# Kernel tuning notes

Hardware: AMD Instinct MI355X
Metric: run time of the kernel (lower is better)

Reference implementation:

```python
import jax, jax.numpy as jnp
import numpy as np

RADIUS = 0.2
NSAMPLE = 32
USE_XYZ = True


def setup_inputs() -> dict:
    key = jax.random.key(0)
    k1, k2, k3 = jax.random.split(key, 3)
    B, N, S, C = 8, 16384, 1024, 64
    xyz = jax.random.uniform(k1, (B, N, 3), dtype=jnp.float32)
    new_xyz = jax.random.uniform(k2, (B, S, 3), dtype=jnp.float32)
    features = jax.random.normal(k3, (B, C, N), dtype=jnp.float32)
    return {"xyz": xyz, "new_xyz": new_xyz, "features": features}


def _ball_query(xyz, new_xyz, radius, nsample):
    """For each query point, the first `nsample` point indices within `radius`,
    padded with the first valid index (0 if none) — matches the CUDA kernel."""
    B, N, _ = xyz.shape
    # squared distances [B, S, N]
    d2 = jnp.sum((new_xyz[:, :, None, :] - xyz[:, None, :, :]) ** 2, axis=-1)
    within = d2 < (radius * radius)
    # encode: valid points keep their index, invalid get sentinel N; sorting
    # then yields the first-in-order valid indices, as the CUDA kernel does.
    keys = jnp.where(within, jnp.arange(N, dtype=jnp.int32)[None, None, :], N)
    idx = jnp.sort(keys, axis=-1)[:, :, :nsample]          # [B, S, K]
    first = idx[:, :, 0:1]
    first = jnp.where(first < N, first, 0)                 # no neighbor -> 0
    idx = jnp.where(idx < N, idx, first)
    return idx.astype(jnp.int32)


def reference(xyz, new_xyz, features):
    idx = _ball_query(xyz, new_xyz, RADIUS, NSAMPLE)       # [B, S, K] int32
    # group xyz: gather [B, S, K, 3] then center on new_xyz
    grouped_xyz = jnp.take_along_axis(xyz[:, None, :, :], idx[:, :, :, None], axis=2)
    grouped_xyz = grouped_xyz - new_xyz[:, :, None, :]
    grouped_xyz = jnp.transpose(grouped_xyz, (0, 3, 1, 2))  # [B, 3, S, K]
    # group features: [B, C, 1, N] gathered with [B, 1, S, K] -> [B, C, S, K]
    grouped_feats = jnp.take_along_axis(features[:, :, :, None].transpose(0, 1, 3, 2),
                                        idx[:, None, :, :], axis=3)
    if USE_XYZ:
        return jnp.concatenate([grouped_xyz, grouped_feats], axis=1)  # [B, 3+C, S, K]
    return grouped_feats
```

## Files before the change

kernel.cpp:

```cpp
#include <hip/hip_runtime.h>


#define BB 8
#define NN 16384
#define SS 1024
#define CC 64
#define NSAMP 32
#define OUTCH (3 + CC)

#define R2 0.04f

__global__ __launch_bounds__(256) void query_kernel(
    const float* __restrict__ xyz,
    const float* __restrict__ new_xyz,
    int* __restrict__ idxq,
    float* __restrict__ out)
{
    __shared__ int sidx[4][NSAMP];

    const int t    = threadIdx.x;
    const int wave = t >> 6;
    const int lane = t & 63;
    const int q    = blockIdx.x * 4 + wave;
    const int b    = q >> 10;
    const int s    = q & (SS - 1);

    const float* xb = xyz + (size_t)b * NN * 3;
    const float qx = new_xyz[((size_t)b * SS + s) * 3 + 0];
    const float qy = new_xyz[((size_t)b * SS + s) * 3 + 1];
    const float qz = new_xyz[((size_t)b * SS + s) * 3 + 2];
    const unsigned long long below = (1ull << lane) - 1ull;

    int count = 0;
    for (int base = 0; base < NN; base += 512) {
        float d2[8];
        #pragma unroll
        for (int j = 0; j < 8; ++j) {
            const int i = base + j * 64 + lane;
            const float dx = qx - xb[i * 3 + 0];
            const float dy = qy - xb[i * 3 + 1];
            const float dz = qz - xb[i * 3 + 2];
            d2[j] = __fadd_rn(__fadd_rn(__fmul_rn(dx, dx),
                                        __fmul_rn(dy, dy)),
                              __fmul_rn(dz, dz));
        }
        #pragma unroll
        for (int j = 0; j < 8; ++j) {
            const bool within = d2[j] < R2;
            const unsigned long long m = __ballot(within);
            if (within) {
                const int pos = count + __popcll(m & below);
                if (pos < NSAMP) sidx[wave][pos] = base + j * 64 + lane;
            }
            count += __popcll(m);
        }
        if (count >= NSAMP) break;
    }
    __syncthreads();
    const int cnt = count < NSAMP ? count : NSAMP;
    const int first = (cnt > 0) ? sidx[wave][0] : 0;
    if (lane < NSAMP && lane >= cnt) sidx[wave][lane] = first;
    __syncthreads();

    if (lane < NSAMP) {
        const int k = lane;
        const int idx = sidx[wave][k];
        idxq[(size_t)q * NSAMP + k] = idx;
        const float gx = xb[idx * 3 + 0] - qx;
        const float gy = xb[idx * 3 + 1] - qy;
        const float gz = xb[idx * 3 + 2] - qz;
        const size_t o = (((size_t)b * OUTCH + 0) * SS + s) * NSAMP + k;
        out[o + 0 * (size_t)SS * NSAMP] = gx;
        out[o + 1 * (size_t)SS * NSAMP] = gy;
        out[o + 2 * (size_t)SS * NSAMP] = gz;
    }
}

__global__ __launch_bounds__(512) void gather_kernel(
    const float* __restrict__ feats,
    const int*   __restrict__ idxq,
    float* __restrict__ out)
{
    __shared__ float row[NN];

    const int c = blockIdx.x;
    const int b = blockIdx.y;
    const int t = threadIdx.x;

    const float* fr = feats + ((size_t)b * CC + c) * NN;
    #pragma unroll
    for (int i = 0; i < 8; ++i) {
        const int o = (i * 512 + t) * 4;
        *(float4*)(row + o) = *(const float4*)(fr + o);
    }
    __syncthreads();

    const int k4 = (t & 7) * 4;
    const int s0 = t >> 3;
    const int*  ib = idxq + (size_t)b * SS * NSAMP;
    float* ob = out + (((size_t)b * OUTCH + 3 + c) * SS) * NSAMP;
    #pragma unroll
    for (int it = 0; it < 16; ++it) {
        const int s = it * 64 + s0;
        const int4 id = *(const int4*)(ib + (size_t)s * NSAMP + k4);
        float4 v;
        v.x = row[id.x];
        v.y = row[id.y];
        v.z = row[id.z];
        v.w = row[id.w];
        *(float4*)(ob + (size_t)s * NSAMP + k4) = v;
    }
}

__global__ __launch_bounds__(64) void qg_fused(
    const float* __restrict__ xyz, const float* __restrict__ new_xyz,
    const float* __restrict__ feats, float* __restrict__ out)
{
    const int bs   = blockIdx.x;
    const int b    = bs >> 10;
    const int s    = bs & (SS - 1);
    const int lane = threadIdx.x;

    const float* xb = xyz + (size_t)b * NN * 3;
    const float qx = new_xyz[((size_t)b * SS + s) * 3 + 0];
    const float qy = new_xyz[((size_t)b * SS + s) * 3 + 1];
    const float qz = new_xyz[((size_t)b * SS + s) * 3 + 2];

    __shared__ int sidx[NSAMP];
    int count = 0;
    for (int base = 0; base < NN; base += 64) {
        const int i = base + lane;
        const float dx = qx - xb[i * 3 + 0];
        const float dy = qy - xb[i * 3 + 1];
        const float dz = qz - xb[i * 3 + 2];
        const float d2 = __fadd_rn(__fadd_rn(__fmul_rn(dx, dx),
                                             __fmul_rn(dy, dy)),
                                   __fmul_rn(dz, dz));
        const bool within = d2 < R2;
        const unsigned long long m = __ballot(within);
        if (within) {
            const int pos = count + __popcll(m & ((1ull << lane) - 1ull));
            if (pos < NSAMP) sidx[pos] = i;
        }
        count += __popcll(m);
        if (count >= NSAMP) break;
    }
    __syncthreads();
    const int cnt = count < NSAMP ? count : NSAMP;
    const int first = (cnt > 0) ? sidx[0] : 0;
    if (lane < NSAMP && lane >= cnt) sidx[lane] = first;
    __syncthreads();

    const int k    = lane & 31;
    const int half = lane >> 5;
    const int idx  = sidx[k];
    const size_t obase = (((size_t)b * OUTCH + 0) * SS + s) * NSAMP + k;
    if (half == 0) {
        out[obase + 0 * (size_t)SS * NSAMP] = xb[idx * 3 + 0] - qx;
        out[obase + 1 * (size_t)SS * NSAMP] = xb[idx * 3 + 1] - qy;
        out[obase + 2 * (size_t)SS * NSAMP] = xb[idx * 3 + 2] - qz;
    }
    const float* fb = feats + (size_t)b * CC * NN;
    const size_t fo = (((size_t)b * OUTCH + 3) * SS + s) * NSAMP + k;
    for (int cch = half; cch < CC; cch += 2) {
        out[fo + (size_t)cch * SS * NSAMP] = fb[(size_t)cch * NN + idx];
    }
}

extern "C" void kernel_launch(void* const* d_in, const int* in_sizes, int n_in,
                              void* d_out, int out_size, void* d_ws, size_t ws_size,
                              hipStream_t stream) {
    const float* xyz     = (const float*)d_in[0];
    const float* new_xyz = (const float*)d_in[1];
    const float* feats   = (const float*)d_in[2];
    float* out           = (float*)d_out;

    const size_t idx_bytes = (size_t)BB * SS * NSAMP * sizeof(int);

    if (ws_size >= idx_bytes) {
        int* idxq = (int*)d_ws;
        query_kernel<<<2048, 256, 0, stream>>>(xyz, new_xyz, idxq, out);
        gather_kernel<<<dim3(CC, BB), 512, 0, stream>>>(feats, idxq, out);
    } else {
        qg_fused<<<BB * SS, 64, 0, stream>>>(xyz, new_xyz, feats, out);
    }
}
```

Before: 115.4 us.

## Use direct global-to-LDS loads, prefetch indices, nontemporal stores, drop block barriers

```diff
diff --git a/kernel.cpp b/kernel.cpp
--- a/kernel.cpp
+++ b/kernel.cpp
@@ -9,6 +9,14 @@
 #define OUTCH (3 + CC)
 
 #define R2 0.04f
+
+typedef float v4f __attribute__((ext_vector_type(4)));
+
+__device__ __forceinline__ void load_lds16(const float* g, float* l) {
+    __builtin_amdgcn_global_load_lds(
+        (const __attribute__((address_space(1))) unsigned int*)g,
+        (__attribute__((address_space(3))) unsigned int*)l, 16, 0, 0);
+}
 
 __global__ __launch_bounds__(256) void query_kernel(
     const float* __restrict__ xyz,
@@ -26,20 +34,20 @@
     const int s    = q & (SS - 1);
 
     const float* xb = xyz + (size_t)b * NN * 3;
+    const float* xl = xb + (size_t)lane * 3;
     const float qx = new_xyz[((size_t)b * SS + s) * 3 + 0];
     const float qy = new_xyz[((size_t)b * SS + s) * 3 + 1];
     const float qz = new_xyz[((size_t)b * SS + s) * 3 + 2];
-    const unsigned long long below = (1ull << lane) - 1ull;
 
     int count = 0;
     for (int base = 0; base < NN; base += 512) {
         float d2[8];
         #pragma unroll
         for (int j = 0; j < 8; ++j) {
-            const int i = base + j * 64 + lane;
-            const float dx = qx - xb[i * 3 + 0];
-            const float dy = qy - xb[i * 3 + 1];
-            const float dz = qz - xb[i * 3 + 2];
+            const float* p = xl + (size_t)(base + j * 64) * 3;
+            const float dx = qx - p[0];
+            const float dy = qy - p[1];
+            const float dz = qz - p[2];
             d2[j] = __fadd_rn(__fadd_rn(__fmul_rn(dx, dx),
                                         __fmul_rn(dy, dy)),
                               __fmul_rn(dz, dz));
@@ -49,18 +57,21 @@
             const bool within = d2[j] < R2;
             const unsigned long long m = __ballot(within);
             if (within) {
-                const int pos = count + __popcll(m & below);
+                const int pre = (int)__builtin_amdgcn_mbcnt_hi(
+                    (unsigned)(m >> 32),
+                    __builtin_amdgcn_mbcnt_lo((unsigned)m, 0u));
+                const int pos = count + pre;
                 if (pos < NSAMP) sidx[wave][pos] = base + j * 64 + lane;
             }
             count += __popcll(m);
         }
         if (count >= NSAMP) break;
     }
-    __syncthreads();
+    asm volatile("s_waitcnt lgkmcnt(0)" ::: "memory");
     const int cnt = count < NSAMP ? count : NSAMP;
     const int first = (cnt > 0) ? sidx[wave][0] : 0;
     if (lane < NSAMP && lane >= cnt) sidx[wave][lane] = first;
-    __syncthreads();
+    asm volatile("s_waitcnt lgkmcnt(0)" ::: "memory");
 
     if (lane < NSAMP) {
         const int k = lane;
@@ -70,13 +81,13 @@
         const float gy = xb[idx * 3 + 1] - qy;
         const float gz = xb[idx * 3 + 2] - qz;
         const size_t o = (((size_t)b * OUTCH + 0) * SS + s) * NSAMP + k;
-        out[o + 0 * (size_t)SS * NSAMP] = gx;
-        out[o + 1 * (size_t)SS * NSAMP] = gy;
-        out[o + 2 * (size_t)SS * NSAMP] = gz;
-    }
-}
-
-__global__ __launch_bounds__(512) void gather_kernel(
+        __builtin_nontemporal_store(gx, out + o + 0 * (size_t)SS * NSAMP);
+        __builtin_nontemporal_store(gy, out + o + 1 * (size_t)SS * NSAMP);
+        __builtin_nontemporal_store(gz, out + o + 2 * (size_t)SS * NSAMP);
+    }
+}
+
+__global__ __launch_bounds__(512, 4) void gather_kernel(
     const float* __restrict__ feats,
     const int*   __restrict__ idxq,
     float* __restrict__ out)
@@ -91,24 +102,30 @@
     #pragma unroll
     for (int i = 0; i < 8; ++i) {
         const int o = (i * 512 + t) * 4;
-        *(float4*)(row + o) = *(const float4*)(fr + o);
-    }
-    __syncthreads();
+        load_lds16(fr + o, row + o);
+    }
 
     const int k4 = (t & 7) * 4;
     const int s0 = t >> 3;
-    const int*  ib = idxq + (size_t)b * SS * NSAMP;
+    const int* ib = idxq + (size_t)b * SS * NSAMP;
+    int4 id[16];
+    #pragma unroll
+    for (int it = 0; it < 16; ++it)
+        id[it] = *(const int4*)(ib + (size_t)(it * 64 + s0) * NSAMP + k4);
+
+    asm volatile("s_waitcnt vmcnt(0)" ::: "memory");
+    __syncthreads();
+
     float* ob = out + (((size_t)b * OUTCH + 3 + c) * SS) * NSAMP;
     #pragma unroll
     for (int it = 0; it < 16; ++it) {
         const int s = it * 64 + s0;
-        const int4 id = *(const int4*)(ib + (size_t)s * NSAMP + k4);
-        float4 v;
-        v.x = row[id.x];
-        v.y = row[id.y];
-        v.z = row[id.z];
-        v.w = row[id.w];
-        *(float4*)(ob + (size_t)s * NSAMP + k4) = v;
+        v4f v;
+        v.x = row[id[it].x];
+        v.y = row[id[it].y];
+        v.z = row[id[it].z];
+        v.w = row[id[it].w];
+        __builtin_nontemporal_store(v, (v4f*)(ob + (size_t)s * NSAMP + k4));
     }
 }
 
```

Result: slower. 121.3 us (+5.1%).
